# Kernel tuning notes

Measured on AMD Instinct MI355X. Metric: run time of the kernel, lower is better.

Reference implementation:

```python
import math
import jax, jax.numpy as jnp
import numpy as np

NUM_NODES = 100000
NUM_EDGES = 1200000
NFEAT, NHID, NCLASS, NLAYER = 128, 64, 16, 4
ALPHA, LAMDA = 0.1, 0.5


def setup_inputs() -> dict:
    key = jax.random.key(0)
    ks = jax.random.split(key, 10)
    x = jax.random.normal(ks[0], (NUM_NODES, NFEAT), dtype=jnp.float32)
    adj_rows = jax.random.randint(ks[1], (NUM_EDGES,), 0, NUM_NODES, dtype=jnp.int32)
    adj_cols = jax.random.randint(ks[2], (NUM_EDGES,), 0, NUM_NODES, dtype=jnp.int32)
    adj_vals = jax.random.uniform(ks[3], (NUM_EDGES,), dtype=jnp.float32)
    # xavier-ish scaled params
    fc0_w = jax.random.normal(ks[4], (NFEAT, NHID), dtype=jnp.float32) * (1.0 / math.sqrt(NFEAT))
    fc0_b = jnp.zeros((NHID,), dtype=jnp.float32)
    conv_w = jax.random.normal(ks[5], (NLAYER, NHID, NHID), dtype=jnp.float32) * 0.02
    conv_b = jnp.zeros((NLAYER, NHID), dtype=jnp.float32)
    fc1_w = jax.random.normal(ks[6], (NHID, NCLASS), dtype=jnp.float32) * (1.0 / math.sqrt(NHID))
    fc1_b = jnp.zeros((NCLASS,), dtype=jnp.float32)
    return {"x": x, "adj_rows": adj_rows, "adj_cols": adj_cols, "adj_vals": adj_vals,
            "fc0_w": fc0_w, "fc0_b": fc0_b, "conv_w": conv_w, "conv_b": conv_b,
            "fc1_w": fc1_w, "fc1_b": fc1_b}


def _spmm(adj_rows, adj_cols, adj_vals, x):
    # sparse [N,N] @ dense [N,d] via gather-multiply-scatter
    msgs = adj_vals[:, None] * x[adj_cols]          # [E, d]
    return jax.ops.segment_sum(msgs, adj_rows, num_segments=NUM_NODES)


def reference(x, adj_rows, adj_cols, adj_vals, fc0_w, fc0_b, conv_w, conv_b, fc1_w, fc1_b):
    # eval mode: dropouts are identity
    h = x @ fc0_w + fc0_b                           # [N, nhid]  (_layers[0], pre-ReLU)
    h0 = h
    li = jax.nn.relu(h)
    for i in range(NLAYER):
        l = i + 1
        theta = math.log(LAMDA / l + 1.0)
        xw = li @ conv_w[i]                         # [N, nhid]
        hi = _spmm(adj_rows, adj_cols, adj_vals, xw)
        support = (1.0 - ALPHA) * hi + ALPHA * h0
        r = support
        out = theta * support + (1.0 - theta) * r + conv_b[i]
        li = jax.nn.relu(out)
    return li @ fc1_w + fc1_b                       # [N, nclass]
```

## Files before the change

### kernel.cpp

```cpp
#include <hip/hip_runtime.h>
#include <hip/hip_bf16.h>

#define NN 100000
#define NE 1200000
#define NF 128
#define NH 64
#define NC 16
#define NB_SCAN 391
#define TILE_R 64
#define NTILES 1563

static __device__ __forceinline__ unsigned short f2bf(float f) {
    __hip_bfloat16 h = __float2bfloat16(f);
    return *reinterpret_cast<unsigned short*>(&h);
}
static __device__ __forceinline__ float bf2f(unsigned short u) {
    __hip_bfloat16 h = *reinterpret_cast<__hip_bfloat16*>(&u);
    return __bfloat162float(h);
}

__global__ __launch_bounds__(256) void zero_deg_kernel(int* __restrict__ deg) {
    int i = blockIdx.x * 256 + threadIdx.x;
    if (i < NN) deg[i] = 0;
}

__global__ __launch_bounds__(256) void hist_kernel(const int* __restrict__ rows,
                                                   int* __restrict__ deg, int nthreads) {
    for (int e = blockIdx.x * 256 + threadIdx.x; e < NE; e += nthreads)
        atomicAdd(&deg[rows[e]], 1);
}

__global__ __launch_bounds__(256) void scan1_kernel(const int* __restrict__ deg,
                                                    int* __restrict__ rs,
                                                    int* __restrict__ blk) {
    __shared__ int sm[256];
    const int tid = threadIdx.x;
    const int i = blockIdx.x * 256 + tid;
    int v = (i < NN) ? deg[i] : 0;
    sm[tid] = v;
    __syncthreads();
#pragma unroll
    for (int off = 1; off < 256; off <<= 1) {
        int t = (tid >= off) ? sm[tid - off] : 0;
        __syncthreads();
        sm[tid] += t;
        __syncthreads();
    }
    if (i < NN) rs[i] = sm[tid] - v;
    if (tid == 255) blk[blockIdx.x] = sm[255];
}

__global__ __launch_bounds__(512) void scan2_kernel(const int* __restrict__ blk,
                                                    int* __restrict__ blk_off) {
    __shared__ int sm[512];
    const int tid = threadIdx.x;
    int v = (tid < NB_SCAN) ? blk[tid] : 0;
    sm[tid] = v;
    __syncthreads();
#pragma unroll
    for (int off = 1; off < 512; off <<= 1) {
        int t = (tid >= off) ? sm[tid - off] : 0;
        __syncthreads();
        sm[tid] += t;
        __syncthreads();
    }
    if (tid < NB_SCAN) blk_off[tid] = sm[tid] - v;
}

__global__ __launch_bounds__(256) void scan3_kernel(int* __restrict__ rs,
                                                    const int* __restrict__ blk_off,
                                                    int* __restrict__ cursor) {
    int i = blockIdx.x * 256 + threadIdx.x;
    if (i < NN) {
        int v = rs[i] + blk_off[i >> 8];
        rs[i] = v;
        cursor[i] = v;
    }
    if (i == 0) rs[NN] = NE;
}

__global__ __launch_bounds__(256) void scatter_kernel(const int* __restrict__ rows,
                                                      const int* __restrict__ cols,
                                                      const float* __restrict__ vals,
                                                      int* __restrict__ cursor,
                                                      int2* __restrict__ packed, int nthreads) {
    for (int e = blockIdx.x * 256 + threadIdx.x; e < NE; e += nthreads) {
        int r = rows[e];
        int pos = atomicAdd(&cursor[r], 1);
        packed[pos] = make_int2(cols[e], __float_as_int(vals[e]));
    }
}

__global__ __launch_bounds__(256) void fc0_kernel(const float* __restrict__ x,
                                                  const float* __restrict__ w,
                                                  const float* __restrict__ b,
                                                  unsigned short* __restrict__ h0) {
    __shared__ float Wl[NF * NH];
    __shared__ float Xt[64 * TILE_R];
    const int tid = threadIdx.x;
    {
        const float4* w4 = (const float4*)w;
        float4* wl4 = (float4*)Wl;
#pragma unroll
        for (int i = tid; i < NF * NH / 4; i += 256) wl4[i] = w4[i];
    }
    const int n0 = blockIdx.x * TILE_R;
    const int c4 = tid & 15;
    const int r4g = tid >> 4;
    const float4 bias = *(const float4*)&b[c4 * 4];
    float acc[4][4];
#pragma unroll
    for (int i = 0; i < 4; ++i) {
        acc[i][0] = bias.x; acc[i][1] = bias.y; acc[i][2] = bias.z; acc[i][3] = bias.w;
    }
    const int lrow = tid & 63;
    const int qbase = tid >> 6;
    const int grow = min(n0 + lrow, NN - 1);
    for (int kk = 0; kk < NF; kk += 64) {
        __syncthreads();
#pragma unroll
        for (int q = qbase; q < 16; q += 4) {
            float4 v = *(const float4*)&x[(size_t)grow * NF + kk + q * 4];
            Xt[(q * 4 + 0) * 64 + lrow] = v.x;
            Xt[(q * 4 + 1) * 64 + lrow] = v.y;
            Xt[(q * 4 + 2) * 64 + lrow] = v.z;
            Xt[(q * 4 + 3) * 64 + lrow] = v.w;
        }
        __syncthreads();
#pragma unroll 8
        for (int k = 0; k < 64; ++k) {
            float4 a4 = *(const float4*)&Xt[k * 64 + r4g * 4];
            float4 w4 = *(const float4*)&Wl[(kk + k) * NH + c4 * 4];
            acc[0][0] = fmaf(a4.x, w4.x, acc[0][0]); acc[0][1] = fmaf(a4.x, w4.y, acc[0][1]);
            acc[0][2] = fmaf(a4.x, w4.z, acc[0][2]); acc[0][3] = fmaf(a4.x, w4.w, acc[0][3]);
            acc[1][0] = fmaf(a4.y, w4.x, acc[1][0]); acc[1][1] = fmaf(a4.y, w4.y, acc[1][1]);
            acc[1][2] = fmaf(a4.y, w4.z, acc[1][2]); acc[1][3] = fmaf(a4.y, w4.w, acc[1][3]);
            acc[2][0] = fmaf(a4.z, w4.x, acc[2][0]); acc[2][1] = fmaf(a4.z, w4.y, acc[2][1]);
            acc[2][2] = fmaf(a4.z, w4.z, acc[2][2]); acc[2][3] = fmaf(a4.z, w4.w, acc[2][3]);
            acc[3][0] = fmaf(a4.w, w4.x, acc[3][0]); acc[3][1] = fmaf(a4.w, w4.y, acc[3][1]);
            acc[3][2] = fmaf(a4.w, w4.z, acc[3][2]); acc[3][3] = fmaf(a4.w, w4.w, acc[3][3]);
        }
    }
#pragma unroll
    for (int i = 0; i < 4; ++i) {
        int row = n0 + r4g * 4 + i;
        if (row < NN) {
            ushort4 o = { f2bf(acc[i][0]), f2bf(acc[i][1]), f2bf(acc[i][2]), f2bf(acc[i][3]) };
            *(ushort4*)&h0[(size_t)row * NH + c4 * 4] = o;
        }
    }
}

template <bool IN_BF16>
__global__ __launch_bounds__(256) void conv_kernel(const void* __restrict__ in_,
                                                   float* __restrict__ xw,
                                                   const float* __restrict__ w) {
    __shared__ float Wl[NH * NH];
    __shared__ float Xt[64 * TILE_R];
    const int tid = threadIdx.x;
    {
        const float4* w4 = (const float4*)w;
        float4* wl4 = (float4*)Wl;
#pragma unroll
        for (int i = tid; i < NH * NH / 4; i += 256) wl4[i] = w4[i];
    }
    const int n0 = blockIdx.x * TILE_R;
    const int lrow = tid & 63;
    const int qbase = tid >> 6;
    const int grow = min(n0 + lrow, NN - 1);
#pragma unroll
    for (int q = qbase; q < 16; q += 4) {
        float e0, e1, e2, e3;
        if constexpr (IN_BF16) {
            ushort4 u = *(const ushort4*)&((const unsigned short*)in_)[(size_t)grow * NH + q * 4];
            e0 = bf2f(u.x); e1 = bf2f(u.y); e2 = bf2f(u.z); e3 = bf2f(u.w);
        } else {
            float4 v = *(const float4*)&((const float*)in_)[(size_t)grow * NH + q * 4];
            e0 = v.x; e1 = v.y; e2 = v.z; e3 = v.w;
        }
        Xt[(q * 4 + 0) * 64 + lrow] = fmaxf(e0, 0.0f);
        Xt[(q * 4 + 1) * 64 + lrow] = fmaxf(e1, 0.0f);
        Xt[(q * 4 + 2) * 64 + lrow] = fmaxf(e2, 0.0f);
        Xt[(q * 4 + 3) * 64 + lrow] = fmaxf(e3, 0.0f);
    }
    __syncthreads();
    const int c4 = tid & 15;
    const int r4g = tid >> 4;
    float acc[4][4];
#pragma unroll
    for (int i = 0; i < 4; ++i)
#pragma unroll
        for (int j = 0; j < 4; ++j) acc[i][j] = 0.0f;
#pragma unroll 8
    for (int k = 0; k < 64; ++k) {
        float4 a4 = *(const float4*)&Xt[k * 64 + r4g * 4];
        float4 w4 = *(const float4*)&Wl[k * NH + c4 * 4];
        acc[0][0] = fmaf(a4.x, w4.x, acc[0][0]); acc[0][1] = fmaf(a4.x, w4.y, acc[0][1]);
        acc[0][2] = fmaf(a4.x, w4.z, acc[0][2]); acc[0][3] = fmaf(a4.x, w4.w, acc[0][3]);
        acc[1][0] = fmaf(a4.y, w4.x, acc[1][0]); acc[1][1] = fmaf(a4.y, w4.y, acc[1][1]);
        acc[1][2] = fmaf(a4.y, w4.z, acc[1][2]); acc[1][3] = fmaf(a4.y, w4.w, acc[1][3]);
        acc[2][0] = fmaf(a4.z, w4.x, acc[2][0]); acc[2][1] = fmaf(a4.z, w4.y, acc[2][1]);
        acc[2][2] = fmaf(a4.z, w4.z, acc[2][2]); acc[2][3] = fmaf(a4.z, w4.w, acc[2][3]);
        acc[3][0] = fmaf(a4.w, w4.x, acc[3][0]); acc[3][1] = fmaf(a4.w, w4.y, acc[3][1]);
        acc[3][2] = fmaf(a4.w, w4.z, acc[3][2]); acc[3][3] = fmaf(a4.w, w4.w, acc[3][3]);
    }
#pragma unroll
    for (int i = 0; i < 4; ++i) {
        int row = n0 + r4g * 4 + i;
        if (row < NN) {
            float4 o = { 0.9f * acc[i][0], 0.9f * acc[i][1], 0.9f * acc[i][2], 0.9f * acc[i][3] };
            *(float4*)&xw[(size_t)row * NH + c4 * 4] = o;
        }
    }
}

__global__ __launch_bounds__(256) void spmm_csr_kernel(const int* __restrict__ rs,
                                                       const int2* __restrict__ packed,
                                                       const float* __restrict__ xw,
                                                       const unsigned short* __restrict__ h0,
                                                       const float* __restrict__ b,
                                                       float* __restrict__ acc,
                                                       int nwaves) {
    const int lane = threadIdx.x & 63;
    const int wid = (blockIdx.x * 256 + threadIdx.x) >> 6;
    const float bias = b[lane];
    for (int n = wid; n < NN; n += nwaves) {
        const int s = rs[n];
        const int e2 = rs[n + 1];
        float a0 = fmaf(0.1f, bf2f(h0[(size_t)n * NH + lane]), bias);
        float a1 = 0.0f, a2 = 0.0f, a3 = 0.0f;
        for (int base = s; base < e2; base += 64) {
            const int cnt = min(64, e2 - base);
            int2 ed = (lane < cnt) ? packed[base + lane] : make_int2(0, 0);
            int j = 0;
            for (; j + 4 <= cnt; j += 4) {
                int c0 = __shfl(ed.x, j);
                int c1 = __shfl(ed.x, j + 1);
                int c2 = __shfl(ed.x, j + 2);
                int c3 = __shfl(ed.x, j + 3);
                float v0 = __int_as_float(__shfl(ed.y, j));
                float v1 = __int_as_float(__shfl(ed.y, j + 1));
                float v2 = __int_as_float(__shfl(ed.y, j + 2));
                float v3 = __int_as_float(__shfl(ed.y, j + 3));
                float g0 = xw[(size_t)c0 * NH + lane];
                float g1 = xw[(size_t)c1 * NH + lane];
                float g2 = xw[(size_t)c2 * NH + lane];
                float g3 = xw[(size_t)c3 * NH + lane];
                a0 = fmaf(v0, g0, a0);
                a1 = fmaf(v1, g1, a1);
                a2 = fmaf(v2, g2, a2);
                a3 = fmaf(v3, g3, a3);
            }
            for (; j < cnt; ++j) {
                int c = __shfl(ed.x, j);
                float v = __int_as_float(__shfl(ed.y, j));
                a0 = fmaf(v, xw[(size_t)c * NH + lane], a0);
            }
        }
        acc[(size_t)n * NH + lane] = (a0 + a1) + (a2 + a3);
    }
}

__global__ __launch_bounds__(256) void fc1_kernel(const float* __restrict__ in,
                                                  const float* __restrict__ w,
                                                  const float* __restrict__ b,
                                                  float* __restrict__ out) {
    __shared__ float Wl[NH * NC];
    __shared__ float Xt[64 * TILE_R];
    const int tid = threadIdx.x;
    for (int i = tid; i < NH * NC; i += 256) Wl[i] = w[i];
    const int n0 = blockIdx.x * TILE_R;
    const int lrow = tid & 63;
    const int qbase = tid >> 6;
    const int grow = min(n0 + lrow, NN - 1);
#pragma unroll
    for (int q = qbase; q < 16; q += 4) {
        float4 v = *(const float4*)&in[(size_t)grow * NH + q * 4];
        Xt[(q * 4 + 0) * 64 + lrow] = fmaxf(v.x, 0.0f);
        Xt[(q * 4 + 1) * 64 + lrow] = fmaxf(v.y, 0.0f);
        Xt[(q * 4 + 2) * 64 + lrow] = fmaxf(v.z, 0.0f);
        Xt[(q * 4 + 3) * 64 + lrow] = fmaxf(v.w, 0.0f);
    }
    __syncthreads();
    const int c = tid & 15;
    const int r4g = tid >> 4;
    float a0 = b[c], a1 = b[c], a2 = b[c], a3 = b[c];
#pragma unroll 8
    for (int k = 0; k < 64; ++k) {
        float4 a4 = *(const float4*)&Xt[k * 64 + r4g * 4];
        float wv = Wl[k * NC + c];
        a0 = fmaf(a4.x, wv, a0);
        a1 = fmaf(a4.y, wv, a1);
        a2 = fmaf(a4.z, wv, a2);
        a3 = fmaf(a4.w, wv, a3);
    }
    int row = n0 + r4g * 4;
    if (row + 0 < NN) out[(size_t)(row + 0) * NC + c] = a0;
    if (row + 1 < NN) out[(size_t)(row + 1) * NC + c] = a1;
    if (row + 2 < NN) out[(size_t)(row + 2) * NC + c] = a2;
    if (row + 3 < NN) out[(size_t)(row + 3) * NC + c] = a3;
}

extern "C" void kernel_launch(void* const* d_in, const int* in_sizes, int n_in,
                              void* d_out, int out_size, void* d_ws, size_t ws_size,
                              hipStream_t stream) {
    const float* x = (const float*)d_in[0];
    const int* rows = (const int*)d_in[1];
    const int* cols = (const int*)d_in[2];
    const float* vals = (const float*)d_in[3];
    const float* fc0_w = (const float*)d_in[4];
    const float* fc0_b = (const float*)d_in[5];
    const float* conv_w = (const float*)d_in[6];
    const float* conv_b = (const float*)d_in[7];
    const float* fc1_w = (const float*)d_in[8];
    const float* fc1_b = (const float*)d_in[9];
    float* out = (float*)d_out;

    char* p = (char*)d_ws;
    unsigned short* h0 = (unsigned short*)p;          p += (size_t)NN * NH * 2;
    float* acc = (float*)p;                           p += (size_t)NN * NH * 4;
    float* xw = (float*)p;                            p += (size_t)NN * NH * 4;
    int2* packed = (int2*)p;                          p += (size_t)NE * 8;
    int* rs = (int*)p;                                p += (size_t)(NN + 1) * 4;
    int* cursor = (int*)p;                            p += (size_t)NN * 4;
    int* deg = (int*)p;                               p += (size_t)NN * 4;
    int* blk = (int*)p;                               p += 512 * 4;
    int* blk_off = (int*)p;                           p += 512 * 4;

    const int nthreads_e = 1200 * 256;
    const int sblocks = 2048;
    const int snwaves = sblocks * 4;

    zero_deg_kernel<<<NB_SCAN, 256, 0, stream>>>(deg);
    hist_kernel<<<1200, 256, 0, stream>>>(rows, deg, nthreads_e);
    scan1_kernel<<<NB_SCAN, 256, 0, stream>>>(deg, rs, blk);
    scan2_kernel<<<1, 512, 0, stream>>>(blk, blk_off);
    scan3_kernel<<<NB_SCAN, 256, 0, stream>>>(rs, blk_off, cursor);
    scatter_kernel<<<1200, 256, 0, stream>>>(rows, cols, vals, cursor, packed, nthreads_e);

    fc0_kernel<<<NTILES, 256, 0, stream>>>(x, fc0_w, fc0_b, h0);

    conv_kernel<true><<<NTILES, 256, 0, stream>>>(h0, xw, conv_w + 0 * NH * NH);
    spmm_csr_kernel<<<sblocks, 256, 0, stream>>>(rs, packed, xw, h0, conv_b + 0 * NH, acc, snwaves);
    for (int i = 1; i < 4; ++i) {
        conv_kernel<false><<<NTILES, 256, 0, stream>>>(acc, xw, conv_w + i * NH * NH);
        spmm_csr_kernel<<<sblocks, 256, 0, stream>>>(rs, packed, xw, h0, conv_b + i * NH, acc, snwaves);
    }

    fc1_kernel<<<NTILES, 256, 0, stream>>>(acc, fc1_w, fc1_b, out);
}
```

Baseline: 559.0 us.

## Store xw in bf16 and partition CSR-build atomics by XCD ownership

The conv output xw is now stored as bf16, which halves the bytes gathered per edge in the SpMM and the bytes written by the conv kernel. Separately, the histogram and scatter kernels split blocks into 8 cohorts keyed on blockIdx&7, and each cohort only performs atomics for rows whose (r>>9)&7 matches it. The aim is to keep atomics to a given row range on one XCD's L2 and avoid cross-die contention. The cost is that every cohort reads the full edge list (8x the row reads), and the extra bf16 rounding of xw reduces precision.

```diff
diff --git a/kernel.cpp b/kernel.cpp
--- a/kernel.cpp
+++ b/kernel.cpp
@@ -25,9 +25,13 @@
 }
 
 __global__ __launch_bounds__(256) void hist_kernel(const int* __restrict__ rows,
-                                                   int* __restrict__ deg, int nthreads) {
-    for (int e = blockIdx.x * 256 + threadIdx.x; e < NE; e += nthreads)
-        atomicAdd(&deg[rows[e]], 1);
+                                                   int* __restrict__ deg, int cohort_threads) {
+    const int xcd = blockIdx.x & 7;
+    const int ctid = (blockIdx.x >> 3) * 256 + threadIdx.x;
+    for (int e = ctid; e < NE; e += cohort_threads) {
+        int r = rows[e];
+        if (((r >> 9) & 7) == xcd) atomicAdd(&deg[r], 1);
+    }
 }
 
 __global__ __launch_bounds__(256) void scan1_kernel(const int* __restrict__ deg,
@@ -83,11 +87,15 @@
                                                       const int* __restrict__ cols,
                                                       const float* __restrict__ vals,
                                                       int* __restrict__ cursor,
-                                                      int2* __restrict__ packed, int nthreads) {
-    for (int e = blockIdx.x * 256 + threadIdx.x; e < NE; e += nthreads) {
+                                                      int2* __restrict__ packed, int cohort_threads) {
+    const int xcd = blockIdx.x & 7;
+    const int ctid = (blockIdx.x >> 3) * 256 + threadIdx.x;
+    for (int e = ctid; e < NE; e += cohort_threads) {
         int r = rows[e];
-        int pos = atomicAdd(&cursor[r], 1);
-        packed[pos] = make_int2(cols[e], __float_as_int(vals[e]));
+        if (((r >> 9) & 7) == xcd) {
+            int pos = atomicAdd(&cursor[r], 1);
+            packed[pos] = make_int2(cols[e], __float_as_int(vals[e]));
+        }
     }
 }
 
@@ -153,7 +161,7 @@
 
 template <bool IN_BF16>
 __global__ __launch_bounds__(256) void conv_kernel(const void* __restrict__ in_,
-                                                   float* __restrict__ xw,
+                                                   unsigned short* __restrict__ xw,
                                                    const float* __restrict__ w) {
     __shared__ float Wl[NH * NH];
     __shared__ float Xt[64 * TILE_R];
@@ -208,15 +216,16 @@
     for (int i = 0; i < 4; ++i) {
         int row = n0 + r4g * 4 + i;
         if (row < NN) {
-            float4 o = { 0.9f * acc[i][0], 0.9f * acc[i][1], 0.9f * acc[i][2], 0.9f * acc[i][3] };
-            *(float4*)&xw[(size_t)row * NH + c4 * 4] = o;
+            ushort4 o = { f2bf(0.9f * acc[i][0]), f2bf(0.9f * acc[i][1]),
+                          f2bf(0.9f * acc[i][2]), f2bf(0.9f * acc[i][3]) };
+            *(ushort4*)&xw[(size_t)row * NH + c4 * 4] = o;
         }
     }
 }
 
 __global__ __launch_bounds__(256) void spmm_csr_kernel(const int* __restrict__ rs,
                                                        const int2* __restrict__ packed,
-                                                       const float* __restrict__ xw,
+                                                       const unsigned short* __restrict__ xw,
                                                        const unsigned short* __restrict__ h0,
                                                        const float* __restrict__ b,
                                                        float* __restrict__ acc,
@@ -242,10 +251,10 @@
                 float v1 = __int_as_float(__shfl(ed.y, j + 1));
                 float v2 = __int_as_float(__shfl(ed.y, j + 2));
                 float v3 = __int_as_float(__shfl(ed.y, j + 3));
-                float g0 = xw[(size_t)c0 * NH + lane];
-                float g1 = xw[(size_t)c1 * NH + lane];
-                float g2 = xw[(size_t)c2 * NH + lane];
-                float g3 = xw[(size_t)c3 * NH + lane];
+                float g0 = bf2f(xw[(size_t)c0 * NH + lane]);
+                float g1 = bf2f(xw[(size_t)c1 * NH + lane]);
+                float g2 = bf2f(xw[(size_t)c2 * NH + lane]);
+                float g3 = bf2f(xw[(size_t)c3 * NH + lane]);
                 a0 = fmaf(v0, g0, a0);
                 a1 = fmaf(v1, g1, a1);
                 a2 = fmaf(v2, g2, a2);
@@ -254,7 +263,7 @@
             for (; j < cnt; ++j) {
                 int c = __shfl(ed.x, j);
                 float v = __int_as_float(__shfl(ed.y, j));
-                a0 = fmaf(v, xw[(size_t)c * NH + lane], a0);
+                a0 = fmaf(v, bf2f(xw[(size_t)c * NH + lane]), a0);
             }
         }
         acc[(size_t)n * NH + lane] = (a0 + a1) + (a2 + a3);
@@ -319,7 +328,7 @@
     char* p = (char*)d_ws;
     unsigned short* h0 = (unsigned short*)p;          p += (size_t)NN * NH * 2;
     float* acc = (float*)p;                           p += (size_t)NN * NH * 4;
-    float* xw = (float*)p;                            p += (size_t)NN * NH * 4;
+    unsigned short* xw = (unsigned short*)p;          p += (size_t)NN * NH * 2;
     int2* packed = (int2*)p;                          p += (size_t)NE * 8;
     int* rs = (int*)p;                                p += (size_t)(NN + 1) * 4;
     int* cursor = (int*)p;                            p += (size_t)NN * 4;
@@ -327,16 +336,17 @@
     int* blk = (int*)p;                               p += 512 * 4;
     int* blk_off = (int*)p;                           p += 512 * 4;
 
-    const int nthreads_e = 1200 * 256;
+    const int ebl = 1200;
+    const int cohort_threads = (ebl / 8) * 256;
     const int sblocks = 2048;
     const int snwaves = sblocks * 4;
 
     zero_deg_kernel<<<NB_SCAN, 256, 0, stream>>>(deg);
-    hist_kernel<<<1200, 256, 0, stream>>>(rows, deg, nthreads_e);
+    hist_kernel<<<ebl, 256, 0, stream>>>(rows, deg, cohort_threads);
     scan1_kernel<<<NB_SCAN, 256, 0, stream>>>(deg, rs, blk);
     scan2_kernel<<<1, 512, 0, stream>>>(blk, blk_off);
     scan3_kernel<<<NB_SCAN, 256, 0, stream>>>(rs, blk_off, cursor);
-    scatter_kernel<<<1200, 256, 0, stream>>>(rows, cols, vals, cursor, packed, nthreads_e);
+    scatter_kernel<<<ebl, 256, 0, stream>>>(rows, cols, vals, cursor, packed, cohort_threads);
 
     fc0_kernel<<<NTILES, 256, 0, stream>>>(x, fc0_w, fc0_b, h0);
 
```

Result: faster. 479.7 us (-14.2%).
